# Kernel optimization log

Hardware: AMD Instinct MI355X
Metric: run time of the kernel (lower is better)

Reference implementation:

```python
import jax, jax.numpy as jnp
import numpy as np

B, C, H, W = 64, 2048, 14, 14
HID, OUT = 2048, 256
NUM_HEADS = 8
SCALE = 1.0
BN_EPS = 1e-5
NORM_EPS = 1e-12


def setup_inputs() -> dict:
    key = jax.random.key(0)
    ks = jax.random.split(key, 5)
    inp = {
        "x": jax.random.normal(ks[0], (B, C, H, W), dtype=jnp.float32),
        # proj MLP1D: conv1(k=1) -> BN -> ReLU -> conv2(k=1), bias=False
        "w1_p": jax.random.normal(ks[1], (HID, C), dtype=jnp.float32) * 0.02,
        "g_p": jnp.ones((HID,), dtype=jnp.float32),
        "b_p": jnp.zeros((HID,), dtype=jnp.float32),
        "w2_p": jax.random.normal(ks[2], (OUT, HID), dtype=jnp.float32) * 0.02,
        # proj_obj MLP1D (same structure)
        "w1_o": jax.random.normal(ks[3], (HID, C), dtype=jnp.float32) * 0.02,
        "g_o": jnp.ones((HID,), dtype=jnp.float32),
        "b_o": jnp.zeros((HID,), dtype=jnp.float32),
        "w2_o": jax.random.normal(ks[4], (OUT, HID), dtype=jnp.float32) * 0.02,
    }
    return inp


def _mlp1d(x, w1, gamma, beta, w2):
    # x: [b, c_in, L]; 1x1 conv == channel matmul
    h = jnp.einsum('oc,bcl->bol', w1, x)  # [b, HID, L]
    # BatchNorm1d, training mode: stats over (batch, length) per channel
    mu = jnp.mean(h, axis=(0, 2), keepdims=True)
    var = jnp.mean(jnp.square(h - mu), axis=(0, 2), keepdims=True)
    h = (h - mu) * jax.lax.rsqrt(var + BN_EPS)
    h = h * gamma[None, :, None] + beta[None, :, None]
    h = jax.nn.relu(h)
    return jnp.einsum('oc,bcl->bol', w2, h)  # [b, OUT, L]


def reference(x, w1_p, g_p, b_p, w2_p, w1_o, g_o, b_o, w2_o):
    b, c, h, w = x.shape
    L = h * w
    xf = x.reshape(b, c, L)                       # [b, c, L]
    x_pool = jnp.mean(xf, axis=2, keepdims=True)  # adaptive_avg_pool2d(1)
    z = _mlp1d(jnp.concatenate([x_pool, xf], axis=2), w1_p, g_p, b_p, w2_p)  # [b, OUT, L+1]
    z_g = z[:, :, :1]          # [b, OUT, 1]
    z_feat = z[:, :, 1:]       # [b, OUT, L]
    # L2 normalize over channel dim, then scale
    nrm = jnp.sqrt(jnp.sum(jnp.square(z_feat), axis=1, keepdims=True))
    a = z_feat / jnp.maximum(nrm, NORM_EPS) / SCALE
    a = a.reshape(b, NUM_HEADS, -1, L)            # [b, H, K, L], K = OUT/H
    obj_attn_raw = jax.nn.softmax(a, axis=-1)
    obj_attn = obj_attn_raw                        # group branch: same softmax
    xh = xf.reshape(b, NUM_HEADS, c // NUM_HEADS, L)
    # matmul(x, attn^T): [b,H,Ch,L] x [b,H,K,L] -> [b,H,Ch,K]
    obj_val = jnp.einsum('bhcl,bhkl->bhck', xh, obj_attn)
    obj_val = obj_val.reshape(b, c, obj_attn.shape[2])  # [b, c, K]
    obj_val = _mlp1d(obj_val, w1_o, g_o, b_o, w2_o)      # [b, OUT, K]
    return (z_g, obj_val, obj_attn, obj_attn_raw)
```

## Files before the change

kernel.cpp:

```cpp
#include <hip/hip_runtime.h>
#include <hip/hip_bf16.h>
#include <math.h>

typedef __bf16 bf16;
typedef bf16 bf16x8 __attribute__((ext_vector_type(8)));
typedef float f32x4 __attribute__((ext_vector_type(4)));

constexpr int BATCH = 64;
constexpr int CIN   = 2048;
constexpr int HIDN  = 2048;
constexpr int OUTN  = 256;
constexpr int LL    = 196;
constexpr int LCAT  = 197;
constexpr int P1V   = BATCH * LCAT;
constexpr int P1P   = 12672;
constexpr size_t O_ZG   = 0;
constexpr size_t O_OVAL = (size_t)BATCH * OUTN;
constexpr size_t O_ATT  = O_OVAL + (size_t)BATCH * OUTN * 32;
constexpr size_t O_ATTR = O_ATT + (size_t)BATCH * OUTN * LL;

constexpr size_t WS_XCAT = 0;
constexpr size_t WS_V2   = WS_XCAT;
constexpr size_t WS_H2T  = WS_XCAT + (size_t)(16u<<20);
constexpr size_t WS_HT   = 51904512;
constexpr size_t WS_Z    = WS_HT + 51904512;
constexpr size_t WS_W1B  = WS_Z + 12976128;
constexpr size_t WS_W2B  = WS_W1B + 8388608;
constexpr size_t WS_W1OB = WS_W2B + 1048576;
constexpr size_t WS_W2OB = WS_W1OB + 8388608;
constexpr size_t WS_NRM  = WS_W2OB + 1048576;
constexpr size_t WS_SUMS = WS_NRM + 50176;
constexpr size_t WS_SC1  = WS_SUMS + 32768;
constexpr size_t WS_SH1  = WS_SC1 + 8192;
constexpr size_t WS_SC2  = WS_SH1 + 8192;
constexpr size_t WS_SH2  = WS_SC2 + 8192;

__global__ __launch_bounds__(256) void cast_k(const float* __restrict__ s, bf16* __restrict__ d, int n){
  int i = blockIdx.x * 256 + threadIdx.x;
  if (i < n) d[i] = (bf16)s[i];
}
__global__ __launch_bounds__(256) void zero_f32(float* p, int n){
  int i = blockIdx.x * 256 + threadIdx.x;
  if (i < n) p[i] = 0.f;
}
__global__ __launch_bounds__(256) void zero_b16(bf16* p, int n){
  int i = blockIdx.x * 256 + threadIdx.x;
  if (i < n) p[i] = (bf16)0.f;
}

__global__ __launch_bounds__(256) void prep_k(const float* __restrict__ x, bf16* __restrict__ xcat){
  __shared__ float xs[LL][66];
  int b  = blockIdx.x >> 5;
  int cg = blockIdx.x & 31;
  int c0 = cg * 64;
  int t  = threadIdx.x;
  const float* xb = x + (size_t)b * CIN * LL + (size_t)c0 * LL;
  for (int cc = 0; cc < 64; cc++){
    if (t < LL) xs[t][cc] = xb[(size_t)cc * LL + t];
  }
  __syncthreads();
  if (t < 64){
    float s = 0.f;
    for (int l = 0; l < LL; l++) s += xs[l][t];
    xcat[(size_t)(b * LCAT) * CIN + c0 + t] = (bf16)(s * (1.f / (float)LL));
  }
  int lw = t >> 6, cc = t & 63;
  for (int i = 0; i < 49; i++){
    int l = i * 4 + lw;
    xcat[(size_t)(b * LCAT + 1 + l) * CIN + c0 + cc] = (bf16)xs[l][cc];
  }
}

__global__ __launch_bounds__(256) void stats_k(const bf16* __restrict__ src, int rows, int rpg,
                                               float* __restrict__ sum, float* __restrict__ sumsq){
  int o  = blockIdx.x * 256 + threadIdx.x;
  int r0 = blockIdx.y * rpg;
  int r1 = min(rows, r0 + rpg);
  float s = 0.f, q = 0.f;
  for (int r = r0; r < r1; r++){
    float v = (float)src[(size_t)r * 2048 + o];
    s += v; q += v * v;
  }
  atomicAdd(&sum[o], s);
  atomicAdd(&sumsq[o], q);
}

__global__ __launch_bounds__(256) void finalize_k(const float* __restrict__ sum, const float* __restrict__ sumsq,
                                                  const float* __restrict__ g, const float* __restrict__ b,
                                                  float n, float* __restrict__ scale, float* __restrict__ shift){
  int o = blockIdx.x * 256 + threadIdx.x;
  float mu  = sum[o] / n;
  float var = sumsq[o] / n - mu * mu;
  float sc  = g[o] / sqrtf(var + 1e-5f);
  scale[o] = sc;
  shift[o] = b[o] - mu * sc;
}

__global__ __launch_bounds__(256) void zg_k(const float* __restrict__ z, float* __restrict__ dout){
  int gidx = blockIdx.x * 256 + threadIdx.x;
  int b = gidx >> 8, c = gidx & 255;
  dout[O_ZG + gidx] = z[(size_t)c * P1P + b * LCAT];
}

__global__ __launch_bounds__(256) void nrm_k(const float* __restrict__ z, float* __restrict__ nrm){
  int b = blockIdx.x, t = threadIdx.x;
  if (t >= LL) return;
  float acc = 0.f;
  const float* zb = z + (size_t)b * LCAT + 1 + t;
  for (int c = 0; c < OUTN; c++){
    float v = zb[(size_t)c * P1P];
    acc += v * v;
  }
  nrm[b * LL + t] = sqrtf(acc);
}

__global__ __launch_bounds__(64) void softmax_k(const float* __restrict__ z, const float* __restrict__ nrm,
                                                float* __restrict__ dout){
  int bc = blockIdx.x;
  int b  = bc >> 8;
  int lane = threadIdx.x;
  const float* zr = z + (size_t)(bc & 255) * P1P + b * LCAT + 1;
  const float* nr = nrm + b * LL;
  float a[4];
  float mx = -1e30f;
  #pragma unroll
  for (int j = 0; j < 4; j++){
    int l = lane + j * 64;
    if (l < LL){
      float v = zr[l] / fmaxf(nr[l], 1e-12f);
      a[j] = v; mx = fmaxf(mx, v);
    } else a[j] = -1e30f;
  }
  #pragma unroll
  for (int s = 1; s < 64; s <<= 1) mx = fmaxf(mx, __shfl_xor(mx, s, 64));
  float sum = 0.f;
  #pragma unroll
  for (int j = 0; j < 4; j++){
    a[j] = (a[j] > -1e29f) ? expf(a[j] - mx) : 0.f;
    sum += a[j];
  }
  #pragma unroll
  for (int s = 1; s < 64; s <<= 1) sum += __shfl_xor(sum, s, 64);
  float inv = 1.f / sum;
  float* o1 = dout + O_ATT  + (size_t)bc * LL;
  float* o2 = dout + O_ATTR + (size_t)bc * LL;
  #pragma unroll
  for (int j = 0; j < 4; j++){
    int l = lane + j * 64;
    if (l < LL){ float r = a[j] * inv; o1[l] = r; o2[l] = r; }
  }
}

template<int CFG>
__global__ __launch_bounds__(256)
void gemm_k(const void* __restrict__ Ap, const void* __restrict__ Qp, void* __restrict__ Cp,
            const float* __restrict__ sc, const float* __restrict__ sh)
{
  constexpr int BM  = (CFG==1 || CFG==3) ? 128 : (CFG==5 ? 32 : 64);
  constexpr int BN  = (CFG==5) ? 256 : 128;
  constexpr int WR  = (CFG==1 || CFG==3) ? 2 : 1;
  constexpr int WC  = 4 / WR;
  constexpr int WTM = BM / WR, WTN = BN / WC;
  constexpr int FM  = WTM / 16, FN = WTN / 16;
  constexpr int KT  = (CFG==5) ? 4 : 32;
  constexpr bool KB   = (CFG==5);
  constexpr bool F32S = (CFG==5);
  constexpr bool QBN  = (CFG==2) || (CFG==4);
  constexpr int LDA = (CFG==5) ? LL : 2048;
  constexpr int LDQ = (CFG==5) ? LL : 2048;
  constexpr int CA  = BM / 32;
  constexpr int CQ  = BN / 32;

  __shared__ bf16 Ps[BM * 64];
  __shared__ bf16 Qs[BN * 64];

  const int t = threadIdx.x;
  const int lane = t & 63;
  const int wid  = t >> 6;
  const int wr = wid / WC, wc = wid % WC;

  size_t aBase = 0, qBase = 0;
  int mOff = 0, nOff = 0;
  if constexpr (CFG == 5){
    int bh = blockIdx.x;
    aBase = (size_t)bh * 32 * LL;
    qBase = ((size_t)(bh >> 3) * 2048 + (size_t)(bh & 7) * 256) * LL;
    mOff = (bh >> 3) * 32;
    nOff = (bh & 7) * 256;
  } else {
    mOff = blockIdx.x * BM;
    nOff = blockIdx.y * BN;
    aBase = (size_t)mOff * LDA;
    qBase = (size_t)nOff * LDQ;
  }

  f32x4 acc[FM][FN] = {};

  for (int kt = 0; kt < KT; ++kt){
    const int k0 = kt * 64;
    bf16x8 ra[CA], rq[CQ];
    #pragma unroll
    for (int i = 0; i < CA; i++){
      int ch = i * 256 + t;
      int row = ch >> 3, kc = ch & 7, kg = k0 + kc * 8;
      if constexpr (F32S){
        const float* g = (const float*)Ap + aBase + (size_t)row * LDA + kg;
        #pragma unroll
        for (int j = 0; j < 8; j++){
          float f = (!KB || (kg + j) < LL) ? g[j] : 0.f;
          ra[i][j] = (bf16)f;
        }
      } else {
        ra[i] = *(const bf16x8*)((const bf16*)Ap + aBase + (size_t)row * LDA + kg);
      }
    }
    #pragma unroll
    for (int i = 0; i < CQ; i++){
      int ch = i * 256 + t;
      int row = ch >> 3, kc = ch & 7, kg = k0 + kc * 8;
      if constexpr (F32S){
        const float* g = (const float*)Qp + qBase + (size_t)row * LDQ + kg;
        #pragma unroll
        for (int j = 0; j < 8; j++){
          float f = ((kg + j) < LL) ? g[j] : 0.f;
          rq[i][j] = (bf16)f;
        }
      } else if constexpr (QBN){
        bf16x8 raw = *(const bf16x8*)((const bf16*)Qp + qBase + (size_t)row * LDQ + kg);
        #pragma unroll
        for (int j = 0; j < 8; j++){
          float f = (float)raw[j] * sc[kg + j] + sh[kg + j];
          rq[i][j] = (bf16)fmaxf(f, 0.f);
        }
      } else {
        rq[i] = *(const bf16x8*)((const bf16*)Qp + qBase + (size_t)row * LDQ + kg);
      }
    }
    __syncthreads();
    #pragma unroll
    for (int i = 0; i < CA; i++){
      int ch = i * 256 + t; int row = ch >> 3, kc = ch & 7;
      *(bf16x8*)&Ps[row * 64 + ((kc ^ (row & 7)) << 3)] = ra[i];
    }
    #pragma unroll
    for (int i = 0; i < CQ; i++){
      int ch = i * 256 + t; int row = ch >> 3, kc = ch & 7;
      *(bf16x8*)&Qs[row * 64 + ((kc ^ (row & 7)) << 3)] = rq[i];
    }
    __syncthreads();
    #pragma unroll
    for (int ks = 0; ks < 2; ++ks){
      const int kcl = ks * 4 + (lane >> 4);
      bf16x8 af[FM], qf[FN];
      #pragma unroll
      for (int m = 0; m < FM; m++){
        int row = wr * WTM + m * 16 + (lane & 15);
        af[m] = *(const bf16x8*)&Ps[row * 64 + ((kcl ^ (row & 7)) << 3)];
      }
      #pragma unroll
      for (int n = 0; n < FN; n++){
        int row = wc * WTN + n * 16 + (lane & 15);
        qf[n] = *(const bf16x8*)&Qs[row * 64 + ((kcl ^ (row & 7)) << 3)];
      }
      #pragma unroll
      for (int m = 0; m < FM; m++)
        #pragma unroll
        for (int n = 0; n < FN; n++)
          acc[m][n] = __builtin_amdgcn_mfma_f32_16x16x32_bf16(af[m], qf[n], acc[m][n], 0, 0, 0);
    }
  }

  #pragma unroll
  for (int m = 0; m < FM; m++){
    #pragma unroll
    for (int n = 0; n < FN; n++){
      #pragma unroll
      for (int r = 0; r < 4; r++){
        int row = mOff + wr * WTM + m * 16 + (lane >> 4) * 4 + r;
        int col = nOff + wc * WTN + n * 16 + (lane & 15);
        float v = acc[m][n][r];
        if constexpr (CFG == 1 || CFG == 3 || CFG == 5){
          ((bf16*)Cp)[(size_t)row * 2048 + col] = (bf16)v;
        } else if constexpr (CFG == 2){
          ((float*)Cp)[(size_t)row * P1P + col] = v;
        } else {
          ((float*)Cp)[O_OVAL + (size_t)(col >> 5) * 8192 + (size_t)row * 32 + (col & 31)] = v;
        }
      }
    }
  }
}

extern "C" void kernel_launch(void* const* d_in, const int* in_sizes, int n_in,
                              void* d_out, int out_size, void* d_ws, size_t ws_size,
                              hipStream_t stream){
  const float* x   = (const float*)d_in[0];
  const float* w1p = (const float*)d_in[1];
  const float* gp  = (const float*)d_in[2];
  const float* bp  = (const float*)d_in[3];
  const float* w2p = (const float*)d_in[4];
  const float* w1o = (const float*)d_in[5];
  const float* go  = (const float*)d_in[6];
  const float* bo  = (const float*)d_in[7];
  const float* w2o = (const float*)d_in[8];
  float* out = (float*)d_out;
  char* ws = (char*)d_ws;

  bf16* xcat = (bf16*)(ws + WS_XCAT);
  bf16* v2   = (bf16*)(ws + WS_V2);
  bf16* h2t  = (bf16*)(ws + WS_H2T);
  bf16* hT   = (bf16*)(ws + WS_HT);
  float* z   = (float*)(ws + WS_Z);
  bf16* w1b  = (bf16*)(ws + WS_W1B);
  bf16* w2b  = (bf16*)(ws + WS_W2B);
  bf16* w1ob = (bf16*)(ws + WS_W1OB);
  bf16* w2ob = (bf16*)(ws + WS_W2OB);
  float* nrmw = (float*)(ws + WS_NRM);
  float* sums = (float*)(ws + WS_SUMS);
  float* sc1 = (float*)(ws + WS_SC1);
  float* sh1 = (float*)(ws + WS_SH1);
  float* sc2 = (float*)(ws + WS_SC2);
  float* sh2 = (float*)(ws + WS_SH2);

  cast_k<<<16384, 256, 0, stream>>>(w1p, w1b, HIDN * CIN);
  cast_k<<<2048,  256, 0, stream>>>(w2p, w2b, OUTN * HIDN);
  cast_k<<<16384, 256, 0, stream>>>(w1o, w1ob, HIDN * CIN);
  cast_k<<<2048,  256, 0, stream>>>(w2o, w2ob, OUTN * HIDN);
  zero_f32<<<32, 256, 0, stream>>>(sums, 4 * 2048);
  zero_b16<<<512, 256, 0, stream>>>(xcat + (size_t)P1V * 2048, (P1P - P1V) * 2048);
  prep_k<<<2048, 256, 0, stream>>>(x, xcat);

  gemm_k<1><<<dim3(99, 16), 256, 0, stream>>>(xcat, w1b, hT, nullptr, nullptr);
  stats_k<<<dim3(8, 32), 256, 0, stream>>>(hT, P1V, 394, sums, sums + 2048);
  finalize_k<<<8, 256, 0, stream>>>(sums, sums + 2048, gp, bp, (float)P1V, sc1, sh1);
  gemm_k<2><<<dim3(4, 99), 256, 0, stream>>>(w2b, hT, z, sc1, sh1);

  zg_k<<<64, 256, 0, stream>>>(z, out);
  nrm_k<<<64, 256, 0, stream>>>(z, nrmw);
  softmax_k<<<16384, 64, 0, stream>>>(z, nrmw, out);

  gemm_k<5><<<512, 256, 0, stream>>>(out + O_ATT, x, v2, nullptr, nullptr);
  gemm_k<3><<<dim3(16, 16), 256, 0, stream>>>(v2, w1ob, h2t, nullptr, nullptr);
  stats_k<<<dim3(8, 8), 256, 0, stream>>>(h2t, 2048, 256, sums + 4096, sums + 6144);
  finalize_k<<<8, 256, 0, stream>>>(sums + 4096, sums + 6144, go, bo, 2048.f, sc2, sh2);
  gemm_k<4><<<dim3(4, 16), 256, 0, stream>>>(w2ob, h2t, out, sc2, sh2);
}
```

Measured before the change: 730.2 us.

## Use direct global-to-LDS loads, XCD block swizzle, vectorized prep/stats, retuned GEMM tiles

The bf16 GEMM operand tiles now go straight from global memory into LDS through global_load_lds with an XOR swizzle. This skips the trip through registers and the separate LDS store. GEMM configs 1 and 3 use a 1D grid remapped so consecutive blocks are spread across XCDs for better L2 locality. Tile shapes for configs 2 and 4 change, prep_k and the fp32 operand loads use float4, and stats_k reads 8 bf16 per thread with fewer blocks. The risks are lower occupancy from fewer stats blocks, and the direct-load path still passing through the same barriers with no explicit wait, which leaves correctness to the compiler's waitcnt handling.

```diff
diff --git a/kernel.cpp b/kernel.cpp
--- a/kernel.cpp
+++ b/kernel.cpp
@@ -35,6 +35,11 @@
 constexpr size_t WS_SC2  = WS_SH1 + 8192;
 constexpr size_t WS_SH2  = WS_SC2 + 8192;
 
+__device__ __forceinline__ void gload16(const bf16* g, bf16* l){
+  __builtin_amdgcn_global_load_lds((const __attribute__((address_space(1))) void*)g,
+                                   (__attribute__((address_space(3))) void*)l, 16, 0, 0);
+}
+
 __global__ __launch_bounds__(256) void cast_k(const float* __restrict__ s, bf16* __restrict__ d, int n){
   int i = blockIdx.x * 256 + threadIdx.x;
   if (i < n) d[i] = (bf16)s[i];
@@ -49,40 +54,51 @@
 }
 
 __global__ __launch_bounds__(256) void prep_k(const float* __restrict__ x, bf16* __restrict__ xcat){
-  __shared__ float xs[LL][66];
+  __shared__ float xs[64][201];
   int b  = blockIdx.x >> 5;
   int cg = blockIdx.x & 31;
   int c0 = cg * 64;
   int t  = threadIdx.x;
-  const float* xb = x + (size_t)b * CIN * LL + (size_t)c0 * LL;
-  for (int cc = 0; cc < 64; cc++){
-    if (t < LL) xs[t][cc] = xb[(size_t)cc * LL + t];
+  const float* xb = x + ((size_t)b * CIN + c0) * LL;
+  #pragma unroll
+  for (int i = 0; i < 16; i++){
+    int idx = i * 256 + t;
+    int cc = idx >> 6, q = idx & 63;
+    if (q < 49){
+      float4 v = *(const float4*)(xb + (size_t)cc * LL + q * 4);
+      xs[cc][q*4+0] = v.x; xs[cc][q*4+1] = v.y; xs[cc][q*4+2] = v.z; xs[cc][q*4+3] = v.w;
+    }
   }
   __syncthreads();
   if (t < 64){
     float s = 0.f;
-    for (int l = 0; l < LL; l++) s += xs[l][t];
+    for (int l = 0; l < LL; l++) s += xs[t][l];
     xcat[(size_t)(b * LCAT) * CIN + c0 + t] = (bf16)(s * (1.f / (float)LL));
   }
   int lw = t >> 6, cc = t & 63;
   for (int i = 0; i < 49; i++){
     int l = i * 4 + lw;
-    xcat[(size_t)(b * LCAT + 1 + l) * CIN + c0 + cc] = (bf16)xs[l][cc];
+    xcat[(size_t)(b * LCAT + 1 + l) * CIN + c0 + cc] = (bf16)xs[cc][l];
   }
 }
 
 __global__ __launch_bounds__(256) void stats_k(const bf16* __restrict__ src, int rows, int rpg,
                                                float* __restrict__ sum, float* __restrict__ sumsq){
-  int o  = blockIdx.x * 256 + threadIdx.x;
-  int r0 = blockIdx.y * rpg;
+  int o  = threadIdx.x * 8;
+  int r0 = blockIdx.x * rpg;
   int r1 = min(rows, r0 + rpg);
-  float s = 0.f, q = 0.f;
+  float s[8] = {0.f,0.f,0.f,0.f,0.f,0.f,0.f,0.f};
+  float q[8] = {0.f,0.f,0.f,0.f,0.f,0.f,0.f,0.f};
   for (int r = r0; r < r1; r++){
-    float v = (float)src[(size_t)r * 2048 + o];
-    s += v; q += v * v;
-  }
-  atomicAdd(&sum[o], s);
-  atomicAdd(&sumsq[o], q);
+    bf16x8 v = *(const bf16x8*)(src + (size_t)r * 2048 + o);
+    #pragma unroll
+    for (int j = 0; j < 8; j++){ float f = (float)v[j]; s[j] += f; q[j] += f * f; }
+  }
+  #pragma unroll
+  for (int j = 0; j < 8; j++){
+    atomicAdd(&sum[o + j], s[j]);
+    atomicAdd(&sumsq[o + j], q[j]);
+  }
 }
 
 __global__ __launch_bounds__(256) void finalize_k(const float* __restrict__ sum, const float* __restrict__ sumsq,
@@ -156,18 +172,19 @@
 void gemm_k(const void* __restrict__ Ap, const void* __restrict__ Qp, void* __restrict__ Cp,
             const float* __restrict__ sc, const float* __restrict__ sh)
 {
-  constexpr int BM  = (CFG==1 || CFG==3) ? 128 : (CFG==5 ? 32 : 64);
-  constexpr int BN  = (CFG==5) ? 256 : 128;
-  constexpr int WR  = (CFG==1 || CFG==3) ? 2 : 1;
+  constexpr int BM  = (CFG==5) ? 32 : (CFG==4 ? 64 : 128);
+  constexpr int BN  = (CFG==5) ? 256 : (CFG==4 ? 64 : 128);
+  constexpr int WR  = (CFG==5) ? 1 : 2;
   constexpr int WC  = 4 / WR;
   constexpr int WTM = BM / WR, WTN = BN / WC;
   constexpr int FM  = WTM / 16, FN = WTN / 16;
   constexpr int KT  = (CFG==5) ? 4 : 32;
-  constexpr bool KB   = (CFG==5);
   constexpr bool F32S = (CFG==5);
   constexpr bool QBN  = (CFG==2) || (CFG==4);
-  constexpr int LDA = (CFG==5) ? LL : 2048;
-  constexpr int LDQ = (CFG==5) ? LL : 2048;
+  constexpr bool AGL  = !F32S;
+  constexpr bool QGL  = (CFG==1) || (CFG==3);
+  constexpr int LDA = F32S ? LL : 2048;
+  constexpr int LDQ = F32S ? LL : 2048;
   constexpr int CA  = BM / 32;
   constexpr int CQ  = BN / 32;
 
@@ -178,6 +195,7 @@
   const int lane = t & 63;
   const int wid  = t >> 6;
   const int wr = wid / WC, wc = wid % WC;
+  const int sw8 = ((lane & 7) ^ (lane >> 3)) * 8;
 
   size_t aBase = 0, qBase = 0;
   int mOff = 0, nOff = 0;
@@ -187,6 +205,16 @@
     qBase = ((size_t)(bh >> 3) * 2048 + (size_t)(bh & 7) * 256) * LL;
     mOff = (bh >> 3) * 32;
     nOff = (bh & 7) * 256;
+  } else if constexpr (CFG == 1){
+    int bid = blockIdx.x;
+    int wg = (bid & 7) * 198 + (bid >> 3);
+    mOff = (wg >> 4) * BM;  nOff = (wg & 15) * BN;
+    aBase = (size_t)mOff * LDA; qBase = (size_t)nOff * LDQ;
+  } else if constexpr (CFG == 3){
+    int bid = blockIdx.x;
+    int wg = (bid & 7) * 32 + (bid >> 3);
+    mOff = (wg >> 4) * BM;  nOff = (wg & 15) * BN;
+    aBase = (size_t)mOff * LDA; qBase = (size_t)nOff * LDQ;
   } else {
     mOff = blockIdx.x * BM;
     nOff = blockIdx.y * BN;
@@ -199,53 +227,81 @@
   for (int kt = 0; kt < KT; ++kt){
     const int k0 = kt * 64;
     bf16x8 ra[CA], rq[CQ];
-    #pragma unroll
-    for (int i = 0; i < CA; i++){
-      int ch = i * 256 + t;
-      int row = ch >> 3, kc = ch & 7, kg = k0 + kc * 8;
-      if constexpr (F32S){
+    if constexpr (!AGL){
+      #pragma unroll
+      for (int i = 0; i < CA; i++){
+        int ch = i * 256 + t;
+        int row = ch >> 3, kc = ch & 7, kg = k0 + kc * 8;
         const float* g = (const float*)Ap + aBase + (size_t)row * LDA + kg;
         #pragma unroll
-        for (int j = 0; j < 8; j++){
-          float f = (!KB || (kg + j) < LL) ? g[j] : 0.f;
-          ra[i][j] = (bf16)f;
+        for (int jj = 0; jj < 8; jj += 4){
+          if (kg + jj + 3 < LL){
+            float4 v = *(const float4*)(g + jj);
+            ra[i][jj] = (bf16)v.x; ra[i][jj+1] = (bf16)v.y;
+            ra[i][jj+2] = (bf16)v.z; ra[i][jj+3] = (bf16)v.w;
+          } else {
+            for (int j = jj; j < jj + 4; j++) ra[i][j] = (bf16)((kg + j) < LL ? g[j] : 0.f);
+          }
         }
-      } else {
-        ra[i] = *(const bf16x8*)((const bf16*)Ap + aBase + (size_t)row * LDA + kg);
-      }
-    }
-    #pragma unroll
-    for (int i = 0; i < CQ; i++){
-      int ch = i * 256 + t;
-      int row = ch >> 3, kc = ch & 7, kg = k0 + kc * 8;
-      if constexpr (F32S){
-        const float* g = (const float*)Qp + qBase + (size_t)row * LDQ + kg;
-        #pragma unroll
-        for (int j = 0; j < 8; j++){
-          float f = ((kg + j) < LL) ? g[j] : 0.f;
-          rq[i][j] = (bf16)f;
+      }
+    }
+    if constexpr (!QGL){
+      #pragma unroll
+      for (int i = 0; i < CQ; i++){
+        int ch = i * 256 + t;
+        int row = ch >> 3, kc = ch & 7, kg = k0 + kc * 8;
+        if constexpr (F32S){
+          const float* g = (const float*)Qp + qBase + (size_t)row * LDQ + kg;
+          #pragma unroll
+          for (int jj = 0; jj < 8; jj += 4){
+            if (kg + jj + 3 < LL){
+              float4 v = *(const float4*)(g + jj);
+              rq[i][jj] = (bf16)v.x; rq[i][jj+1] = (bf16)v.y;
+              rq[i][jj+2] = (bf16)v.z; rq[i][jj+3] = (bf16)v.w;
+            } else {
+              for (int j = jj; j < jj + 4; j++) rq[i][j] = (bf16)((kg + j) < LL ? g[j] : 0.f);
+            }
+          }
+        } else {
+          bf16x8 raw = *(const bf16x8*)((const bf16*)Qp + qBase + (size_t)row * LDQ + kg);
+          #pragma unroll
+          for (int j = 0; j < 8; j++){
+            float f = (float)raw[j] * sc[kg + j] + sh[kg + j];
+            rq[i][j] = (bf16)fmaxf(f, 0.f);
+          }
         }
-      } else if constexpr (QBN){
-        bf16x8 raw = *(const bf16x8*)((const bf16*)Qp + qBase + (size_t)row * LDQ + kg);
-        #pragma unroll
-        for (int j = 0; j < 8; j++){
-          float f = (float)raw[j] * sc[kg + j] + sh[kg + j];
-          rq[i][j] = (bf16)fmaxf(f, 0.f);
-        }
-      } else {
-        rq[i] = *(const bf16x8*)((const bf16*)Qp + qBase + (size_t)row * LDQ + kg);
       }
     }
     __syncthreads();
-    #pragma unroll
-    for (int i = 0; i < CA; i++){
-      int ch = i * 256 + t; int row = ch >> 3, kc = ch & 7;
-      *(bf16x8*)&Ps[row * 64 + ((kc ^ (row & 7)) << 3)] = ra[i];
-    }
-    #pragma unroll
-    for (int i = 0; i < CQ; i++){
-      int ch = i * 256 + t; int row = ch >> 3, kc = ch & 7;
-      *(bf16x8*)&Qs[row * 64 + ((kc ^ (row & 7)) << 3)] = rq[i];
+    if constexpr (AGL){
+      #pragma unroll
+      for (int c = 0; c < CA; c++){
+        int chunk = wid * CA + c;
+        int row = chunk * 8 + (lane >> 3);
+        gload16((const bf16*)Ap + aBase + (size_t)row * LDA + k0 + sw8, &Ps[chunk * 512]);
+      }
+    }
+    if constexpr (QGL){
+      #pragma unroll
+      for (int c = 0; c < CQ; c++){
+        int chunk = wid * CQ + c;
+        int row = chunk * 8 + (lane >> 3);
+        gload16((const bf16*)Qp + qBase + (size_t)row * LDQ + k0 + sw8, &Qs[chunk * 512]);
+      }
+    }
+    if constexpr (!AGL){
+      #pragma unroll
+      for (int i = 0; i < CA; i++){
+        int ch = i * 256 + t; int row = ch >> 3, kc = ch & 7;
+        *(bf16x8*)&Ps[row * 64 + ((kc ^ (row & 7)) << 3)] = ra[i];
+      }
+    }
+    if constexpr (!QGL){
+      #pragma unroll
+      for (int i = 0; i < CQ; i++){
+        int ch = i * 256 + t; int row = ch >> 3, kc = ch & 7;
+        *(bf16x8*)&Qs[row * 64 + ((kc ^ (row & 7)) << 3)] = rq[i];
+      }
     }
     __syncthreads();
     #pragma unroll
@@ -330,18 +386,18 @@
   zero_b16<<<512, 256, 0, stream>>>(xcat + (size_t)P1V * 2048, (P1P - P1V) * 2048);
   prep_k<<<2048, 256, 0, stream>>>(x, xcat);
 
-  gemm_k<1><<<dim3(99, 16), 256, 0, stream>>>(xcat, w1b, hT, nullptr, nullptr);
-  stats_k<<<dim3(8, 32), 256, 0, stream>>>(hT, P1V, 394, sums, sums + 2048);
+  gemm_k<1><<<1584, 256, 0, stream>>>(xcat, w1b, hT, nullptr, nullptr);
+  stats_k<<<32, 256, 0, stream>>>(hT, P1V, 394, sums, sums + 2048);
   finalize_k<<<8, 256, 0, stream>>>(sums, sums + 2048, gp, bp, (float)P1V, sc1, sh1);
-  gemm_k<2><<<dim3(4, 99), 256, 0, stream>>>(w2b, hT, z, sc1, sh1);
+  gemm_k<2><<<dim3(2, 99), 256, 0, stream>>>(w2b, hT, z, sc1, sh1);
 
   zg_k<<<64, 256, 0, stream>>>(z, out);
   nrm_k<<<64, 256, 0, stream>>>(z, nrmw);
   softmax_k<<<16384, 64, 0, stream>>>(z, nrmw, out);
 
   gemm_k<5><<<512, 256, 0, stream>>>(out + O_ATT, x, v2, nullptr, nullptr);
-  gemm_k<3><<<dim3(16, 16), 256, 0, stream>>>(v2, w1ob, h2t, nullptr, nullptr);
-  stats_k<<<dim3(8, 8), 256, 0, stream>>>(h2t, 2048, 256, sums + 4096, sums + 6144);
+  gemm_k<3><<<256, 256, 0, stream>>>(v2, w1ob, h2t, nullptr, nullptr);
+  stats_k<<<8, 256, 0, stream>>>(h2t, 2048, 256, sums + 4096, sums + 6144);
   finalize_k<<<8, 256, 0, stream>>>(sums + 4096, sums + 6144, go, bo, 2048.f, sc2, sh2);
-  gemm_k<4><<<dim3(4, 16), 256, 0, stream>>>(w2ob, h2t, out, sc2, sh2);
-}
+  gemm_k<4><<<dim3(4, 32), 256, 0, stream>>>(w2ob, h2t, out, sc2, sh2);
+}
```

Measured after the change: 730.5 us. No clear change (+0.0%).
